# Optimization experiments

Measured on AMD Instinct MI355X. Metric: run time of the kernel, lower is better.

## Reference

```python
import jax, jax.numpy as jnp
import numpy as np

DROP_P = 0.2  # ligru_drop for the single layer


def qweight(w):
    """Build the (4*in_q, 4*out_q) Hamilton-product block matrix from stacked
    component weights w of shape (4, in_q, out_q) ordered (r, i, j, k)."""
    r, i, j, k = w[0], w[1], w[2], w[3]
    c_r = jnp.concatenate([r, -i, -j, -k], axis=0)
    c_i = jnp.concatenate([i,  r, -k,  j], axis=0)
    c_j = jnp.concatenate([j,  k,  r, -i], axis=0)
    c_k = jnp.concatenate([k, -j,  i,  r], axis=0)
    return jnp.concatenate([c_r, c_i, c_j, c_k], axis=1)


def setup_inputs() -> dict:
    key = jax.random.key(0)
    ks = jax.random.split(key, 6)
    T, B, F, H = 1000, 32, 1024, 1024
    s = np.float32(1.0 / np.sqrt(F))  # glorot-ish scale to keep recurrence stable
    x = jax.random.normal(ks[0], (T, B, F), dtype=jnp.float32)
    wh_w = jax.random.normal(ks[1], (4, F // 4, H // 4), dtype=jnp.float32) * s
    wz_w = jax.random.normal(ks[2], (4, F // 4, H // 4), dtype=jnp.float32) * s
    uh_w = jax.random.normal(ks[3], (4, H // 4, H // 4), dtype=jnp.float32) * s
    uz_w = jax.random.normal(ks[4], (4, H // 4, H // 4), dtype=jnp.float32) * s
    wh_b = jnp.zeros((H,), jnp.float32)
    wz_b = jnp.zeros((H,), jnp.float32)
    # train-mode bernoulli dropout mask, fixed across time (as in the torch code)
    drop_mask = (jax.random.uniform(ks[5], (B, H)) < (1.0 - DROP_P)).astype(jnp.float32)
    return {"x": x, "wh_w": wh_w, "wh_b": wh_b, "wz_w": wz_w, "wz_b": wz_b,
            "uh_w": uh_w, "uz_w": uz_w, "drop_mask": drop_mask}


def reference(x, wh_w, wh_b, wz_w, wz_b, uh_w, uz_w, drop_mask):
    # x: (T, B, F)
    Wh, Wz = qweight(wh_w), qweight(wz_w)  # (F, H)
    Uh, Uz = qweight(uh_w), qweight(uz_w)  # (H, H)
    # precompute input projections across all timesteps (big GEMMs)
    wh_out = jnp.einsum('tbf,fh->tbh', x, Wh) + wh_b
    wz_out = jnp.einsum('tbf,fh->tbh', x, Wz) + wz_b
    h0 = jnp.zeros((x.shape[1], Uh.shape[1]), x.dtype)

    def step(ht, inp):
        wh_t, wz_t = inp
        zt = jax.nn.sigmoid(wz_t + ht @ Uz)
        at = wh_t + ht @ Uh
        hcand = jax.nn.relu(at) * drop_mask
        ht = zt * ht + (1.0 - zt) * hcand
        return ht, ht

    _, h = jax.lax.scan(step, h0, (wh_out, wz_out))  # h: (T, B, H)
    return h
```

## Files before the change

kernel.cpp:

```cpp
#include <hip/hip_runtime.h>
#include <stdint.h>

typedef unsigned short u16;
typedef __attribute__((ext_vector_type(8))) __bf16 bf16x8;
typedef __attribute__((ext_vector_type(4))) float f32x4;

#define NBLK 64
#define TSTEPS 1000

__device__ __forceinline__ u16 f2bf(float f) {
    uint32_t u = __builtin_bit_cast(uint32_t, f);
    u += 0x7fffu + ((u >> 16) & 1u);
    return (u16)(u >> 16);
}
__device__ __forceinline__ float bf2f(u16 s) {
    uint32_t u = ((uint32_t)s) << 16;
    return __builtin_bit_cast(float, u);
}

__device__ __forceinline__ void store_u16_sc(u16* p, u16 v) {
    asm volatile("global_store_short %0, %1, off sc0 sc1"
                 :: "v"(p), "v"((uint32_t)v) : "memory");
}

__device__ const int   q_comp[4][4] = {{0,1,2,3},{1,0,3,2},{2,3,0,1},{3,2,1,0}};
__device__ const float q_sgn [4][4] = {{ 1.f, 1.f, 1.f, 1.f},
                                       {-1.f, 1.f, 1.f,-1.f},
                                       {-1.f,-1.f, 1.f, 1.f},
                                       {-1.f, 1.f,-1.f, 1.f}};

__global__ void k_convert_x(const float* __restrict__ x, u16* __restrict__ xb, int n8) {
    int i = blockIdx.x * blockDim.x + threadIdx.x;
    if (i >= n8) return;
    const float4* p = (const float4*)x;
    float4 v0 = p[2*i], v1 = p[2*i + 1];
    u16 o[8];
    o[0]=f2bf(v0.x); o[1]=f2bf(v0.y); o[2]=f2bf(v0.z); o[3]=f2bf(v0.w);
    o[4]=f2bf(v1.x); o[5]=f2bf(v1.y); o[6]=f2bf(v1.z); o[7]=f2bf(v1.w);
    *(uint4*)(xb + (size_t)i*8) = *(uint4*)o;
}

__global__ void k_build_wq(const float* __restrict__ wh_w, const float* __restrict__ wz_w,
                           u16* __restrict__ wqT) {
    int tid = blockIdx.x * blockDim.x + threadIdx.x;
    int n = tid >> 7, kg = tid & 127;
    const float* src = (n < 1024) ? wh_w : wz_w;
    int nn = n & 1023;
    int cj = nn >> 8, b = nn & 255;
    int k0 = kg << 3;
    int ci = k0 >> 8, a0 = k0 & 255;
    int c = q_comp[ci][cj];
    float s = q_sgn[ci][cj];
    const float* sp = src + c*65536 + a0*256 + b;
    u16 o[8];
    #pragma unroll
    for (int e = 0; e < 8; ++e) o[e] = f2bf(s * sp[e*256]);
    *(uint4*)(wqT + (size_t)n*1024 + k0) = *(uint4*)o;
}

__global__ void k_build_upack(const float* __restrict__ uh_w, const float* __restrict__ uz_w,
                              u16* __restrict__ upack) {
    int tid = blockIdx.x * blockDim.x + threadIdx.x;
    int l   = tid & 63;
    int ks  = (tid >> 6) & 31;
    int nt  = (tid >> 11) & 1;
    int blk = tid >> 12;
    int j   = (blk << 4) + (l & 15);
    int k0  = (ks << 5) + ((l >> 4) << 3);
    int ci = k0 >> 8, a0 = k0 & 255;
    int cj = j >> 8, b = j & 255;
    const float* src = nt ? uz_w : uh_w;
    int c = q_comp[ci][cj];
    float s = q_sgn[ci][cj];
    const float* sp = src + c*65536 + a0*256 + b;
    u16 o[8];
    #pragma unroll
    for (int e = 0; e < 8; ++e) o[e] = f2bf(s * sp[e*256]);
    *(uint4*)(upack + (size_t)tid*8) = *(uint4*)o;
}

__global__ __launch_bounds__(256) void k_gemm(
        const u16* __restrict__ A, const u16* __restrict__ Bt,
        const float* __restrict__ whb, const float* __restrict__ wzb,
        u16* __restrict__ C)
{
    __shared__ __align__(16) u16 lsA[128*32];
    __shared__ __align__(16) u16 lsB[128*32];
    int bid = blockIdx.x;
    int swz = (bid & 7) * 500 + (bid >> 3);
    int mi = swz >> 4, ni = swz & 15;
    int m0 = mi << 7, n0 = ni << 7;
    int tid = threadIdx.x;
    int w = tid >> 6, l = tid & 63;
    int wm = w >> 1, wn = w & 1;
    f32x4 acc[4][4];
    #pragma unroll
    for (int i = 0; i < 4; ++i)
        #pragma unroll
        for (int j = 0; j < 4; ++j) acc[i][j] = (f32x4){0.f,0.f,0.f,0.f};

    for (int kt = 0; kt < 32; ++kt) {
        int k0 = kt << 5;
        #pragma unroll
        for (int r = 0; r < 2; ++r) {
            int c = r*256 + w*64 + l;
            const u16* ga = A + (size_t)(m0 + (c >> 2))*1024 + k0 + (c & 3)*8;
            __builtin_amdgcn_global_load_lds(
                (const __attribute__((address_space(1))) uint32_t*)ga,
                (__attribute__((address_space(3))) uint32_t*)((char*)lsA + r*4096 + w*1024),
                16, 0, 0);
            const u16* gb = Bt + (size_t)(n0 + (c >> 2))*1024 + k0 + (c & 3)*8;
            __builtin_amdgcn_global_load_lds(
                (const __attribute__((address_space(1))) uint32_t*)gb,
                (__attribute__((address_space(3))) uint32_t*)((char*)lsB + r*4096 + w*1024),
                16, 0, 0);
        }
        __syncthreads();
        uint4 af[4], bfr[4];
        #pragma unroll
        for (int i = 0; i < 4; ++i) {
            int rowa = wm*64 + i*16 + (l & 15);
            af[i]  = *(const uint4*)((const char*)lsA + rowa*64 + (l >> 4)*16);
            int rowb = wn*64 + i*16 + (l & 15);
            bfr[i] = *(const uint4*)((const char*)lsB + rowb*64 + (l >> 4)*16);
        }
        #pragma unroll
        for (int i = 0; i < 4; ++i)
            #pragma unroll
            for (int j = 0; j < 4; ++j)
                acc[i][j] = __builtin_amdgcn_mfma_f32_16x16x32_bf16(
                    __builtin_bit_cast(bf16x8, af[i]),
                    __builtin_bit_cast(bf16x8, bfr[j]),
                    acc[i][j], 0, 0, 0);
        __syncthreads();
    }
    #pragma unroll
    for (int j = 0; j < 4; ++j) {
        int col = n0 + wn*64 + j*16 + (l & 15);
        float bias = (col < 1024) ? whb[col] : wzb[col - 1024];
        #pragma unroll
        for (int i = 0; i < 4; ++i) {
            int rowm = m0 + wm*64 + i*16 + ((l >> 4) << 2);
            #pragma unroll
            for (int q = 0; q < 4; ++q)
                C[(size_t)(rowm + q)*2048 + col] = f2bf(acc[i][j][q] + bias);
        }
    }
}

__global__ __launch_bounds__(128) void k_rec(
        const u16* __restrict__ upack,
        u16* __restrict__ hbuf,
        uint32_t* __restrict__ flags,
        const float* __restrict__ drop,
        float* __restrict__ out)
{
    __shared__ __align__(16) uint4 ubs[4096];
    const int tid = threadIdx.x;
    const int blk = blockIdx.x;
    const int mt = tid >> 6, l = tid & 63;
    const int wid = (blk << 1) + mt;

    const uint4* ug = (const uint4*)upack + (size_t)blk*4096;
    #pragma unroll 4
    for (int r = 0; r < 32; ++r) ubs[r*128 + tid] = ug[r*128 + tid];

    const int j  = (blk << 4) + (l & 15);
    const int b0 = (mt << 4) + ((l >> 4) << 2);
    float h[4] = {0.f,0.f,0.f,0.f};
    float dm[4];
    #pragma unroll
    for (int q = 0; q < 4; ++q) dm[q] = drop[(b0 + q)*1024 + j];

    const u16* pj = (const u16*)out;
    u16 whu[4], wzu[4];
    #pragma unroll
    for (int q = 0; q < 4; ++q) {
        size_t row = (size_t)(b0 + q) * 2048;
        whu[q] = pj[row + j];
        wzu[q] = pj[row + 1024 + j];
    }
    const int hoff = ((mt*32 + (j >> 5))*64 + (((j >> 3) & 3)*16 + ((l >> 4) << 2)))*8 + (j & 7);

    __syncthreads();

    for (int t = 0; t < TSTEPS; ++t) {
        u16 nwh[4], nwz[4];
        if (t < TSTEPS - 1) {
            #pragma unroll
            for (int q = 0; q < 4; ++q) {
                size_t row = (size_t)((t + 1)*32 + b0 + q) * 2048;
                nwh[q] = pj[row + j];
                nwz[q] = pj[row + 1024 + j];
            }
        }

        if (t > 0) {
            bool ok;
            do {
                unsigned long long v = __hip_atomic_load(
                    (const unsigned long long*)(flags + 2*l),
                    __ATOMIC_RELAXED, __HIP_MEMORY_SCOPE_AGENT);
                ok = ((uint32_t)v >= (uint32_t)t) && ((uint32_t)(v >> 32) >= (uint32_t)t);
            } while (!__all(ok));
            asm volatile("" ::: "memory");
            __builtin_amdgcn_sched_barrier(0);
        }

        const u16* hb  = hbuf + ((t & 1) << 15);
        u16*       hbn = hbuf + (((t + 1) & 1) << 15);

        f32x4 acch = {0.f,0.f,0.f,0.f}, accz = {0.f,0.f,0.f,0.f};
        #pragma unroll
        for (int ks = 0; ks < 32; ++ks) {
            const u16* p = hb + (((mt*32 + ks)*64 + l) << 3);
            unsigned long long lo = __hip_atomic_load((const unsigned long long*)p,
                __ATOMIC_RELAXED, __HIP_MEMORY_SCOPE_AGENT);
            unsigned long long hi = __hip_atomic_load((const unsigned long long*)(p + 4),
                __ATOMIC_RELAXED, __HIP_MEMORY_SCOPE_AGENT);
            uint4 av4 = {(uint32_t)lo, (uint32_t)(lo >> 32),
                         (uint32_t)hi, (uint32_t)(hi >> 32)};
            bf16x8 av = __builtin_bit_cast(bf16x8, av4);
            bf16x8 bh = __builtin_bit_cast(bf16x8, ubs[ks*64 + l]);
            bf16x8 bz = __builtin_bit_cast(bf16x8, ubs[(32 + ks)*64 + l]);
            acch = __builtin_amdgcn_mfma_f32_16x16x32_bf16(av, bh, acch, 0, 0, 0);
            accz = __builtin_amdgcn_mfma_f32_16x16x32_bf16(av, bz, accz, 0, 0, 0);
        }

        const size_t orow = (size_t)t << 15;
        #pragma unroll
        for (int q = 0; q < 4; ++q) {
            float a  = acch[q] + bf2f(whu[q]);
            float zl = accz[q] + bf2f(wzu[q]);
            float z  = 1.0f / (1.0f + __expf(-zl));
            float hc = fmaxf(a, 0.0f) * dm[q];
            float hn = z * h[q] + (1.0f - z) * hc;
            h[q] = hn;
            out[orow + (size_t)(b0 + q)*1024 + j] = hn;
            store_u16_sc(hbn + hoff + (q << 3), f2bf(hn));
        }
        if (t < TSTEPS - 1) {
            #pragma unroll
            for (int q = 0; q < 4; ++q) { whu[q] = nwh[q]; wzu[q] = nwz[q]; }
        }

        asm volatile("s_waitcnt vmcnt(0)" ::: "memory");
        if (l == 0)
            __hip_atomic_store(&flags[wid], (uint32_t)(t + 1),
                               __ATOMIC_RELAXED, __HIP_MEMORY_SCOPE_AGENT);
    }
}

extern "C" void kernel_launch(void* const* d_in, const int* in_sizes, int n_in,
                              void* d_out, int out_size, void* d_ws, size_t ws_size,
                              hipStream_t stream) {
    const float* x    = (const float*)d_in[0];
    const float* wh_w = (const float*)d_in[1];
    const float* wh_b = (const float*)d_in[2];
    const float* wz_w = (const float*)d_in[3];
    const float* wz_b = (const float*)d_in[4];
    const float* uh_w = (const float*)d_in[5];
    const float* uz_w = (const float*)d_in[6];
    const float* drop = (const float*)d_in[7];

    char* ws = (char*)d_ws;
    u16*      xb    = (u16*)ws;
    u16*      wqT   = (u16*)(ws + 65536000);
    u16*      upack = (u16*)(ws + 65536000 + 4194304);
    u16*      hbuf  = (u16*)(ws + 65536000 + 8388608);
    uint32_t* flg   = (uint32_t*)(ws + 65536000 + 8388608 + 131072);

    hipMemsetAsync(flg, 0, 4096, stream);
    hipMemsetAsync(hbuf, 0, 65536, stream);

    k_convert_x  <<<16000, 256, 0, stream>>>(x, xb, 4096000);
    k_build_wq   <<<1024, 256, 0, stream>>>(wh_w, wz_w, wqT);
    k_build_upack<<<1024, 256, 0, stream>>>(uh_w, uz_w, upack);
    k_gemm       <<<4000, 256, 0, stream>>>(xb, wqT, wh_b, wz_b, (u16*)d_out);
    k_rec        <<<NBLK, 128, 0, stream>>>(upack, hbuf, flg, drop, (float*)d_out);
}
```

Measured before the change: 4.852 ms.

## Restructure recurrence step: batched h loads, LDS-transposed vector publish, packed 16-bit flags

Each step now issues all 32 hidden-state loads as dwordx4 cache-bypassing loads up front, along with the projection prefetch, then waits once. The old code instead did paired 64-bit atomic loads inside the MFMA loop. New h values are staged in LDS and published with one coalesced dwordx4 store per lane instead of scattered short stores. Per-wave flags shrink to 16-bit halves so one 32-bit load checks two producers. The MFMA chain is split into two accumulators, and the fp32 output store is deferred by one step to take it off the critical path. The aim is to cut per-step latency of the serial recurrence. The costs are more registers, an extra LDS round trip, and subtle ordering assumptions about the aliased output/projection buffer.

Measured after the change: 6.429 ms. 32.5% more time.

```diff
diff --git a/kernel.cpp b/kernel.cpp
--- a/kernel.cpp
+++ b/kernel.cpp
@@ -4,6 +4,7 @@
 typedef unsigned short u16;
 typedef __attribute__((ext_vector_type(8))) __bf16 bf16x8;
 typedef __attribute__((ext_vector_type(4))) float f32x4;
+typedef __attribute__((ext_vector_type(4))) uint32_t u32x4;
 
 #define NBLK 64
 #define TSTEPS 1000
@@ -16,11 +17,6 @@
 __device__ __forceinline__ float bf2f(u16 s) {
     uint32_t u = ((uint32_t)s) << 16;
     return __builtin_bit_cast(float, u);
-}
-
-__device__ __forceinline__ void store_u16_sc(u16* p, u16 v) {
-    asm volatile("global_store_short %0, %1, off sc0 sc1"
-                 :: "v"(p), "v"((uint32_t)v) : "memory");
 }
 
 __device__ const int   q_comp[4][4] = {{0,1,2,3},{1,0,3,2},{2,3,0,1},{3,2,1,0}};
@@ -148,14 +144,21 @@
     }
 }
 
-__global__ __launch_bounds__(128) void k_rec(
+
+#define PF(Q) \
+    asm volatile("global_load_ushort %0, %2, off\n\t" \
+                 "global_load_ushort %1, %2, off offset:2048" \
+                 : "=v"(nwh[Q]), "=v"(nwz[Q]) : "v"(pa + (Q)*4096) : "memory");
+
+__global__ __launch_bounds__(128, 1) void k_rec(
         const u16* __restrict__ upack,
-        u16* __restrict__ hbuf,
+        u16* __restrict__ hb,
         uint32_t* __restrict__ flags,
         const float* __restrict__ drop,
         float* __restrict__ out)
 {
     __shared__ __align__(16) uint4 ubs[4096];
+    __shared__ __align__(16) u16 tx[512];
     const int tid = threadIdx.x;
     const int blk = blockIdx.x;
     const int mt = tid >> 6, l = tid & 63;
@@ -167,87 +170,108 @@
 
     const int j  = (blk << 4) + (l & 15);
     const int b0 = (mt << 4) + ((l >> 4) << 2);
-    float h[4] = {0.f,0.f,0.f,0.f};
+    float h[4]    = {0.f,0.f,0.f,0.f};
+    float pout[4] = {0.f,0.f,0.f,0.f};
     float dm[4];
     #pragma unroll
     for (int q = 0; q < 4; ++q) dm[q] = drop[(b0 + q)*1024 + j];
 
     const u16* pj = (const u16*)out;
-    u16 whu[4], wzu[4];
+    uint32_t whu[4], wzu[4];
     #pragma unroll
     for (int q = 0; q < 4; ++q) {
-        size_t row = (size_t)(b0 + q) * 2048;
-        whu[q] = pj[row + j];
-        wzu[q] = pj[row + 1024 + j];
-    }
-    const int hoff = ((mt*32 + (j >> 5))*64 + (((j >> 3) & 3)*16 + ((l >> 4) << 2)))*8 + (j & 7);
+        size_t rowp = (size_t)(b0 + q) * 2048;
+        whu[q] = pj[rowp + j];
+        wzu[q] = pj[rowp + 1024 + j];
+    }
+    const uint32_t cb  = (uint32_t)(mt*32768 + l*16);
+    const uint32_t pbb = (uint32_t)((mt*32 + (blk >> 1))*1024 + (blk & 1)*512 + (l & 31)*16);
 
     __syncthreads();
 
     for (int t = 0; t < TSTEPS; ++t) {
-        u16 nwh[4], nwz[4];
-        if (t < TSTEPS - 1) {
-            #pragma unroll
-            for (int q = 0; q < 4; ++q) {
-                size_t row = (size_t)((t + 1)*32 + b0 + q) * 2048;
-                nwh[q] = pj[row + j];
-                nwz[q] = pj[row + 1024 + j];
-            }
-        }
-
-        if (t > 0) {
+        {
+            uint32_t fv;
             bool ok;
             do {
-                unsigned long long v = __hip_atomic_load(
-                    (const unsigned long long*)(flags + 2*l),
-                    __ATOMIC_RELAXED, __HIP_MEMORY_SCOPE_AGENT);
-                ok = ((uint32_t)v >= (uint32_t)t) && ((uint32_t)(v >> 32) >= (uint32_t)t);
+                fv = __hip_atomic_load(&flags[l], __ATOMIC_RELAXED, __HIP_MEMORY_SCOPE_AGENT);
+                ok = ((fv & 0xFFFFu) >= (uint32_t)t) && ((fv >> 16) >= (uint32_t)t);
             } while (!__all(ok));
-            asm volatile("" ::: "memory");
-            __builtin_amdgcn_sched_barrier(0);
-        }
-
-        const u16* hb  = hbuf + ((t & 1) << 15);
-        u16*       hbn = hbuf + (((t + 1) & 1) << 15);
-
-        f32x4 acch = {0.f,0.f,0.f,0.f}, accz = {0.f,0.f,0.f,0.f};
+        }
+
+        u32x4 hv[32];
+        const char* cp = (const char*)hb + ((t & 1) << 16) + cb;
+        #pragma unroll
+        for (int ks = 0; ks < 32; ++ks)
+            asm volatile("global_load_dwordx4 %0, %1, off sc0 sc1"
+                         : "=v"(hv[ks]) : "v"(cp + ks*1024) : "memory");
+        uint32_t nwh[4], nwz[4];
+        if (t < TSTEPS - 1) {
+            const char* pa = (const char*)pj + ((((size_t)(t + 1) << 5) + b0)*2048 + j)*2;
+            PF(0) PF(1) PF(2) PF(3)
+        }
+        asm volatile("s_waitcnt vmcnt(0)" ::: "memory");
+        __builtin_amdgcn_sched_barrier(0);
+
+        f32x4 acch0 = {0.f,0.f,0.f,0.f}, acch1 = {0.f,0.f,0.f,0.f};
+        f32x4 accz0 = {0.f,0.f,0.f,0.f}, accz1 = {0.f,0.f,0.f,0.f};
         #pragma unroll
         for (int ks = 0; ks < 32; ++ks) {
-            const u16* p = hb + (((mt*32 + ks)*64 + l) << 3);
-            unsigned long long lo = __hip_atomic_load((const unsigned long long*)p,
-                __ATOMIC_RELAXED, __HIP_MEMORY_SCOPE_AGENT);
-            unsigned long long hi = __hip_atomic_load((const unsigned long long*)(p + 4),
-                __ATOMIC_RELAXED, __HIP_MEMORY_SCOPE_AGENT);
-            uint4 av4 = {(uint32_t)lo, (uint32_t)(lo >> 32),
-                         (uint32_t)hi, (uint32_t)(hi >> 32)};
-            bf16x8 av = __builtin_bit_cast(bf16x8, av4);
+            bf16x8 av = __builtin_bit_cast(bf16x8, hv[ks]);
             bf16x8 bh = __builtin_bit_cast(bf16x8, ubs[ks*64 + l]);
             bf16x8 bz = __builtin_bit_cast(bf16x8, ubs[(32 + ks)*64 + l]);
-            acch = __builtin_amdgcn_mfma_f32_16x16x32_bf16(av, bh, acch, 0, 0, 0);
-            accz = __builtin_amdgcn_mfma_f32_16x16x32_bf16(av, bz, accz, 0, 0, 0);
-        }
-
-        const size_t orow = (size_t)t << 15;
+            if (ks & 1) {
+                acch1 = __builtin_amdgcn_mfma_f32_16x16x32_bf16(av, bh, acch1, 0, 0, 0);
+                accz1 = __builtin_amdgcn_mfma_f32_16x16x32_bf16(av, bz, accz1, 0, 0, 0);
+            } else {
+                acch0 = __builtin_amdgcn_mfma_f32_16x16x32_bf16(av, bh, acch0, 0, 0, 0);
+                accz0 = __builtin_amdgcn_mfma_f32_16x16x32_bf16(av, bz, accz0, 0, 0, 0);
+            }
+        }
+
+        f32x4 acch = acch0 + acch1, accz = accz0 + accz1;
+        u16* txw = tx + mt*256;
         #pragma unroll
         for (int q = 0; q < 4; ++q) {
-            float a  = acch[q] + bf2f(whu[q]);
-            float zl = accz[q] + bf2f(wzu[q]);
+            float a  = acch[q] + bf2f((u16)whu[q]);
+            float zl = accz[q] + bf2f((u16)wzu[q]);
             float z  = 1.0f / (1.0f + __expf(-zl));
             float hc = fmaxf(a, 0.0f) * dm[q];
             float hn = z * h[q] + (1.0f - z) * hc;
             h[q] = hn;
-            out[orow + (size_t)(b0 + q)*1024 + j] = hn;
-            store_u16_sc(hbn + hoff + (q << 3), f2bf(hn));
-        }
+            txw[(((l >> 4)*4 + q)*8) + ((l & 15) >> 3)*128 + (l & 7)] = f2bf(hn);
+        }
+
+        if (l < 32) {
+            u32x4 pubv = *(const u32x4*)((const char*)tx + mt*512 + l*16);
+            char* pp = (char*)hb + (((t + 1) & 1) << 16) + pbb;
+            asm volatile("global_store_dwordx4 %0, %1, off sc0 sc1"
+                         :: "v"(pp), "v"(pubv) : "memory");
+        }
+        asm volatile("s_waitcnt vmcnt(0)" ::: "memory");
+        if (l == 0) {
+            u16* fp = (u16*)flags + wid;
+            asm volatile("global_store_short %0, %1, off sc0 sc1"
+                         :: "v"(fp), "v"((uint32_t)(t + 1)) : "memory");
+        }
+
+        if (t > 0) {
+            float* ob = out + (((size_t)(t - 1)) << 15) + (size_t)b0*1024 + j;
+            #pragma unroll
+            for (int q = 0; q < 4; ++q) ob[q*1024] = pout[q];
+        }
+        #pragma unroll
+        for (int q = 0; q < 4; ++q) pout[q] = h[q];
         if (t < TSTEPS - 1) {
             #pragma unroll
             for (int q = 0; q < 4; ++q) { whu[q] = nwh[q]; wzu[q] = nwz[q]; }
         }
-
-        asm volatile("s_waitcnt vmcnt(0)" ::: "memory");
-        if (l == 0)
-            __hip_atomic_store(&flags[wid], (uint32_t)(t + 1),
-                               __ATOMIC_RELAXED, __HIP_MEMORY_SCOPE_AGENT);
+    }
+
+    {
+        float* ob = out + (((size_t)(TSTEPS - 1)) << 15) + (size_t)b0*1024 + j;
+        #pragma unroll
+        for (int q = 0; q < 4; ++q) ob[q*1024] = pout[q];
     }
 }
 
@@ -267,15 +291,15 @@
     u16*      xb    = (u16*)ws;
     u16*      wqT   = (u16*)(ws + 65536000);
     u16*      upack = (u16*)(ws + 65536000 + 4194304);
-    u16*      hbuf  = (u16*)(ws + 65536000 + 8388608);
+    u16*      hb    = (u16*)(ws + 65536000 + 8388608);
     uint32_t* flg   = (uint32_t*)(ws + 65536000 + 8388608 + 131072);
 
-    hipMemsetAsync(flg, 0, 4096, stream);
-    hipMemsetAsync(hbuf, 0, 65536, stream);
+    (void)hipMemsetAsync(flg, 0, 256, stream);
+    (void)hipMemsetAsync(hb, 0, 65536, stream);
 
     k_convert_x  <<<16000, 256, 0, stream>>>(x, xb, 4096000);
     k_build_wq   <<<1024, 256, 0, stream>>>(wh_w, wz_w, wqT);
     k_build_upack<<<1024, 256, 0, stream>>>(uh_w, uz_w, upack);
     k_gemm       <<<4000, 256, 0, stream>>>(xb, wqT, wh_b, wz_b, (u16*)d_out);
-    k_rec        <<<NBLK, 128, 0, stream>>>(upack, hbuf, flg, drop, (float*)d_out);
-}
+    k_rec        <<<NBLK, 128, 0, stream>>>(upack, hb, flg, drop, (float*)d_out);
+}
```
